# Optimization experiments

Hardware: AMD Instinct MI355X
Metric: run time of the kernel (lower is better)

Reference implementation:

```python
import jax, jax.numpy as jnp
import numpy as np

B, N, D, H = 16, 256, 128, 8
HD = D // H
PAIR_DIMS = [64, 64, 64]
EPS = 1e-8


def _pairwise_lv_fts(x):
    # x: [B, 4, N] four-vectors (px, py, pz, E); returns [B, N, N, 4] = (lnkt, lnz, lndelta, lnm2)
    px, py, pz, e = x[:, 0], x[:, 1], x[:, 2], x[:, 3]
    pt = jnp.sqrt(jnp.clip(px ** 2 + py ** 2, EPS))          # [B, N]
    rap = 0.5 * jnp.log1p(2.0 * pz / jnp.clip(e - pz, 1e-20))
    phi = jnp.arctan2(py, px)
    d_rap = rap[:, :, None] - rap[:, None, :]                 # [B, N, N]
    d_phi = (phi[:, :, None] - phi[:, None, :] + np.pi) % (2.0 * np.pi) - np.pi
    delta = jnp.sqrt(d_rap ** 2 + d_phi ** 2)
    lndelta = jnp.log(jnp.clip(delta, EPS))
    ptmin = jnp.minimum(pt[:, :, None], pt[:, None, :])
    lnkt = jnp.log(jnp.clip(ptmin * delta, EPS))
    lnz = jnp.log(jnp.clip(ptmin / jnp.clip(pt[:, :, None] + pt[:, None, :], EPS), EPS))
    es = e[:, :, None] + e[:, None, :]
    pxs = px[:, :, None] + px[:, None, :]
    pys = py[:, :, None] + py[:, None, :]
    pzs = pz[:, :, None] + pz[:, None, :]
    lnm2 = jnp.log(jnp.clip(es ** 2 - pxs ** 2 - pys ** 2 - pzs ** 2, EPS))
    return jnp.stack([lnkt, lnz, lndelta, lnm2], axis=-1)


def setup_inputs() -> dict:
    key = jax.random.key(0)
    ks = jax.random.split(key, 12)
    p3 = jax.random.normal(ks[0], (B, 3, N), jnp.float32)
    e = jnp.sqrt((p3 ** 2).sum(1, keepdims=True)
                 + jnp.abs(jax.random.normal(ks[1], (B, 1, N), jnp.float32)) ** 2 + 0.1)
    x_pf = jnp.concatenate([p3, e], axis=1)                   # physical four-vectors [B,4,N]
    x_feat = jax.random.normal(ks[2], (B, N, D), jnp.float32) * 0.02
    dims = [4] + PAIR_DIMS + [H]
    pw = {}
    for i in range(4):
        pw[f"pair_w{i}"] = jax.random.normal(ks[3 + i], (dims[i], dims[i + 1]), jnp.float32) / np.sqrt(dims[i])
        pw[f"pair_b{i}"] = jnp.zeros((dims[i + 1],), jnp.float32)
    proj = {n: jax.random.normal(k, (D, D), jnp.float32) / np.sqrt(D)
            for n, k in zip(["wq", "wk", "wv", "wo"], jax.random.split(ks[7], 4))}
    bias = {n: jnp.zeros((D,), jnp.float32) for n in ["bq", "bk", "bv", "bo"]}
    return dict(x_pf=x_pf, x_feat=x_feat, **pw, **proj, **bias)


def reference(x_pf, x_feat, pair_w0, pair_b0, pair_w1, pair_b1, pair_w2, pair_b2,
              pair_w3, pair_b3, wq, wk, wv, wo, bq, bk, bv, bo):
    # pairwise Lorentz-invariant features -> dense attention bias
    u = _pairwise_lv_fts(x_pf)                                # [B, N, N, 4]
    for w, b in ((pair_w0, pair_b0), (pair_w1, pair_b1), (pair_w2, pair_b2)):
        u = jax.nn.gelu(u @ w + b)
    attn_bias = jnp.transpose(u @ pair_w3 + pair_b3, (0, 3, 1, 2))  # [B, H, N, N]
    # multi-head attention with pairwise bias
    q = (x_feat @ wq + bq).reshape(B, N, H, HD)
    k = (x_feat @ wk + bk).reshape(B, N, H, HD)
    v = (x_feat @ wv + bv).reshape(B, N, H, HD)
    scores = jnp.einsum("bihd,bjhd->bhij", q, k) / np.sqrt(HD) + attn_bias
    attn = jax.nn.softmax(scores, axis=-1)
    out = jnp.einsum("bhij,bjhd->bihd", attn, v).reshape(B, N, D)
    return out @ wo + bo                                      # [B, N, D]
```

## Files before the change

### kernel.cpp

```cpp
#include <hip/hip_runtime.h>
#include <hip/hip_bf16.h>
#include <math.h>

#define B_ 16
#define N_ 256
#define D_ 128
#define H_ 8
#define HD_ 16
#define EPS_ 1e-8f
#define PI_F 3.14159265358979323846f
#define TWO_PI_F 6.28318530717958647692f
#define INV_TWO_PI_F 0.15915494309189533577f
#define L2E_F 1.4426950408889634f

#define OFF_PT   0
#define OFF_RAP  4096
#define OFF_PHI  8192
#define OFF_PX   12288
#define OFF_PY   16384
#define OFF_PZ   20480
#define OFF_E    24576
#define OFF_Q    28672
#define OFF_K    (28672 + 524288)
#define OFF_V    (28672 + 2*524288)
#define OFF_BIAS (28672 + 3*524288)
#define OFF_AO   (OFF_BIAS + 8388608)
#define OFF_WPACK (OFF_AO + 524288)

#define UA0  0
#define UA1H 2048
#define UA1L 6144
#define UA2H 10240
#define UA2L 14336
#define UA3H 18432
#define UA3L 19456
#define UQKV 20480

typedef _Float16 f16x8 __attribute__((ext_vector_type(8)));
typedef _Float16 f16x4 __attribute__((ext_vector_type(4)));
typedef _Float16 f16x2 __attribute__((ext_vector_type(2)));
typedef __attribute__((ext_vector_type(4))) float f4;
typedef __attribute__((ext_vector_type(4))) unsigned int u4;

__device__ __forceinline__ unsigned pkh2(float a, float b) {
    f16x2 v = { (_Float16)a, (_Float16)b };
    return __builtin_bit_cast(unsigned, v);
}
__device__ __forceinline__ float f16res(float x) {
    return x - (float)(_Float16)x;
}

__device__ __forceinline__ float gelu_f(float x) {
    float y2 = x * fmaf(0.10294337f, x * x, 2.3022079f);
    float e = __builtin_amdgcn_exp2f(-y2);
    return x * __builtin_amdgcn_rcpf(1.0f + e);
}


__global__ __launch_bounds__(256) void k_prep(
    const float* __restrict__ w0, const float* __restrict__ w1,
    const float* __restrict__ w2, const float* __restrict__ w3,
    const float* __restrict__ wq, const float* __restrict__ wk,
    const float* __restrict__ wv, const float* __restrict__ wo,
    _Float16* __restrict__ wp) {
    int id0 = blockIdx.x * 256 + threadIdx.x;
    int gs = gridDim.x * 256;
    for (int e = id0; e < 2048; e += gs) {
        int fi = e >> 3, j = e & 7;
        int mt = fi >> 6, lane = fi & 63;
        int q = lane >> 4, ln = lane & 15;
        int m = mt * 16 + ln;
        _Float16 v = (_Float16)0.0f;
        if (q == 0) v = (j < 4) ? (_Float16)w0[j * 64 + m]
                                : (_Float16)f16res(w0[(j - 4) * 64 + m]);
        else if (q == 1) v = (j < 4) ? (_Float16)w0[j * 64 + m] : (_Float16)0.0f;
        wp[UA0 + e] = v;
    }
    for (int e = id0; e < 4096; e += gs) {
        int fi = e >> 3, j = e & 7;
        int mt = fi >> 7, ks = (fi >> 6) & 1, lane = fi & 63;
        int q = lane >> 4;
        int m = mt * 16 + (lane & 15);
        int k = (2 * (j >> 2) + ks) * 16 + q * 4 + (j & 3);
        float x1 = w1[k * 64 + m];
        wp[UA1H + e] = (_Float16)x1;
        wp[UA1L + e] = (_Float16)f16res(x1);
        float x2 = w2[k * 64 + m];
        wp[UA2H + e] = (_Float16)x2;
        wp[UA2L + e] = (_Float16)f16res(x2);
    }
    for (int e = id0; e < 1024; e += gs) {
        int fi = e >> 3, j = e & 7;
        int ks = fi >> 6, lane = fi & 63;
        int q = lane >> 4;
        int m = lane & 15;
        int k = (2 * (j >> 2) + ks) * 16 + q * 4 + (j & 3);
        float x = (m < 8) ? w3[k * 8 + m] : 0.0f;
        wp[UA3H + e] = (_Float16)x;
        wp[UA3L + e] = (_Float16)f16res(x);
    }
    const float* mats[4] = { wq, wk, wv, wo };
#pragma unroll 1
    for (int mi = 0; mi < 4; ++mi) {
        const float* W = mats[mi];
        _Float16* dst = wp + UQKV + mi * 32768;
        for (int e = id0; e < 16384; e += gs) {
            int fi = e >> 3, j = e & 7;
            int mt = fi >> 8, ks = (fi >> 6) & 3, lane = fi & 63;
            int k = ks * 32 + ((lane >> 4) << 3) + j;
            int o = mt * 16 + (lane & 15);
            float x = W[k * 128 + o];
            dst[e] = (_Float16)x;
            dst[16384 + e] = (_Float16)f16res(x);
        }
    }
}

__global__ __launch_bounds__(256) void k_particle(const float* __restrict__ x_pf,
                                                  float* __restrict__ ws) {
    int idx = blockIdx.x * 256 + threadIdx.x;
    int b = idx >> 8, n = idx & 255;
    const float* base = x_pf + (size_t)b * 4 * N_;
    float px = base[0 * N_ + n];
    float py = base[1 * N_ + n];
    float pz = base[2 * N_ + n];
    float e  = base[3 * N_ + n];
    float pt  = sqrtf(fmaxf(px * px + py * py, EPS_));
    float rap = 0.5f * log1pf(2.0f * pz / fmaxf(e - pz, 1e-20f));
    float phi = atan2f(py, px);
    ws[OFF_PT  + idx] = pt;
    ws[OFF_RAP + idx] = rap;
    ws[OFF_PHI + idx] = phi;
    ws[OFF_PX  + idx] = px;
    ws[OFF_PY  + idx] = py;
    ws[OFF_PZ  + idx] = pz;
    ws[OFF_E   + idx] = e;
}

__device__ __forceinline__ void epi_frag(const f4 (&acc)[4][4], const float* __restrict__ bg,
                                         int q, u4 (&Bu)[4][2]) {
#pragma unroll
    for (int mt = 0; mt < 4; ++mt) {
        f4 bv = *(const f4*)&bg[mt * 16 + q * 4];
        int ks = mt & 1, hi = (mt >> 1) * 2;
#pragma unroll
        for (int nt = 0; nt < 4; ++nt) {
            float g0 = gelu_f(acc[mt][nt][0] + bv[0]);
            float g1 = gelu_f(acc[mt][nt][1] + bv[1]);
            float g2 = gelu_f(acc[mt][nt][2] + bv[2]);
            float g3 = gelu_f(acc[mt][nt][3] + bv[3]);
            Bu[nt][ks][hi]     = pkh2(g0, g1);
            Bu[nt][ks][hi + 1] = pkh2(g2, g3);
        }
    }
}

__device__ __forceinline__ void mid_layer(f4 (&acc)[4][4],
                                          const _Float16* __restrict__ wh,
                                          const _Float16* __restrict__ wl,
                                          int lane, const u4 (&Bu)[4][2]) {
    const f4 zero4 = { 0.f, 0.f, 0.f, 0.f };
#pragma unroll
    for (int mt = 0; mt < 4; ++mt) {
        f16x8 ah0 = *(const f16x8*)&wh[((mt * 2 + 0) * 64 + lane) * 8];
        f16x8 ah1 = *(const f16x8*)&wh[((mt * 2 + 1) * 64 + lane) * 8];
        f16x8 al0 = *(const f16x8*)&wl[((mt * 2 + 0) * 64 + lane) * 8];
        f16x8 al1 = *(const f16x8*)&wl[((mt * 2 + 1) * 64 + lane) * 8];
#pragma unroll
        for (int nt = 0; nt < 4; ++nt) {
            f16x8 b0 = __builtin_bit_cast(f16x8, Bu[nt][0]);
            f16x8 b1 = __builtin_bit_cast(f16x8, Bu[nt][1]);
            f4 c = zero4;
            c = __builtin_amdgcn_mfma_f32_16x16x32_f16(ah0, b0, c, 0, 0, 0);
            c = __builtin_amdgcn_mfma_f32_16x16x32_f16(al0, b0, c, 0, 0, 0);
            c = __builtin_amdgcn_mfma_f32_16x16x32_f16(ah1, b1, c, 0, 0, 0);
            c = __builtin_amdgcn_mfma_f32_16x16x32_f16(al1, b1, c, 0, 0, 0);
            acc[mt][nt] = c;
        }
    }
}

__global__ __launch_bounds__(256, 4) void k_pair_mlp(
    const float* __restrict__ ws, const _Float16* __restrict__ wp,
    const float* __restrict__ b0g, const float* __restrict__ b1g,
    const float* __restrict__ b2g, const float* __restrict__ b3g,
    float* __restrict__ bias_out) {
    int tid = threadIdx.x;
    int lane = tid & 63;
    int ln = lane & 15, q = lane >> 4;
    int wid = blockIdx.x * 4 + (tid >> 6);
    int row = wid >> 2;
    int j0 = (wid & 3) * 64;
    int b = row >> 8, i = row & 255;

    unsigned FH01, FH23, FL01, FL23;
    {
        int ib = row;
        int jb = (b << 8) + j0 + lane;
        float pt_i = ws[OFF_PT + ib],  rap_i = ws[OFF_RAP + ib], phi_i = ws[OFF_PHI + ib];
        float px_i = ws[OFF_PX + ib],  py_i  = ws[OFF_PY  + ib];
        float pz_i = ws[OFF_PZ + ib],  e_i   = ws[OFF_E   + ib];
        float pt_j = ws[OFF_PT + jb],  rap_j = ws[OFF_RAP + jb], phi_j = ws[OFF_PHI + jb];
        float px_j = ws[OFF_PX + jb],  py_j  = ws[OFF_PY  + jb];
        float pz_j = ws[OFF_PZ + jb],  e_j   = ws[OFF_E   + jb];

        float drap = rap_i - rap_j;
        float xw = phi_i - phi_j + PI_F;
        float mw = xw - TWO_PI_F * floorf(xw * INV_TWO_PI_F);
        float dphi = mw - PI_F;
        float delta = sqrtf(drap * drap + dphi * dphi);
        float f2 = __logf(fmaxf(delta, EPS_));
        float ptmin = fminf(pt_i, pt_j);
        float f0 = __logf(fmaxf(ptmin * delta, EPS_));
        float f1 = __logf(fmaxf(ptmin / fmaxf(pt_i + pt_j, EPS_), EPS_));
        float es = e_i + e_j, pxs = px_i + px_j, pys = py_i + py_j, pzs = pz_i + pz_j;
        float f3 = __logf(fmaxf(es * es - pxs * pxs - pys * pys - pzs * pzs, EPS_));

        FH01 = pkh2(f0, f1);
        FH23 = pkh2(f2, f3);
        FL01 = pkh2(f16res(f0), f16res(f1));
        FL23 = pkh2(f16res(f2), f16res(f3));
    }

    f4 acc[4][4];
    const f4 zero4 = { 0.f, 0.f, 0.f, 0.f };

    {
        f16x8 a0[4];
#pragma unroll
        for (int mt = 0; mt < 4; ++mt)
            a0[mt] = *(const f16x8*)&wp[UA0 + (mt * 64 + lane) * 8];
#pragma unroll
        for (int nt = 0; nt < 4; ++nt) {
            int src = nt * 16 + ln;
            unsigned h01 = (unsigned)__shfl((int)FH01, src);
            unsigned h23 = (unsigned)__shfl((int)FH23, src);
            unsigned l01 = (unsigned)__shfl((int)FL01, src);
            unsigned l23 = (unsigned)__shfl((int)FL23, src);
            u4 bu;
            bu[0] = (q == 0) ? h01 : ((q == 1) ? l01 : 0u);
            bu[1] = (q == 0) ? h23 : ((q == 1) ? l23 : 0u);
            bu[2] = (q == 0) ? h01 : 0u;
            bu[3] = (q == 0) ? h23 : 0u;
            f16x8 bf = __builtin_bit_cast(f16x8, bu);
#pragma unroll
            for (int mt = 0; mt < 4; ++mt)
                acc[mt][nt] = __builtin_amdgcn_mfma_f32_16x16x32_f16(a0[mt], bf, zero4, 0, 0, 0);
        }
    }

    u4 Bu[4][2];
    epi_frag(acc, b0g, q, Bu);
    mid_layer(acc, wp + UA1H, wp + UA1L, lane, Bu);
    epi_frag(acc, b1g, q, Bu);
    mid_layer(acc, wp + UA2H, wp + UA2L, lane, Bu);
    epi_frag(acc, b2g, q, Bu);

    {
        f16x8 a3h0 = *(const f16x8*)&wp[UA3H + (0 * 64 + lane) * 8];
        f16x8 a3h1 = *(const f16x8*)&wp[UA3H + (1 * 64 + lane) * 8];
        f16x8 a3l0 = *(const f16x8*)&wp[UA3L + (0 * 64 + lane) * 8];
        f16x8 a3l1 = *(const f16x8*)&wp[UA3L + (1 * 64 + lane) * 8];
        f4 acc3[4];
#pragma unroll
        for (int nt = 0; nt < 4; ++nt) {
            f16x8 b0 = __builtin_bit_cast(f16x8, Bu[nt][0]);
            f16x8 b1 = __builtin_bit_cast(f16x8, Bu[nt][1]);
            f4 c = zero4;
            c = __builtin_amdgcn_mfma_f32_16x16x32_f16(a3h0, b0, c, 0, 0, 0);
            c = __builtin_amdgcn_mfma_f32_16x16x32_f16(a3l0, b0, c, 0, 0, 0);
            c = __builtin_amdgcn_mfma_f32_16x16x32_f16(a3h1, b1, c, 0, 0, 0);
            c = __builtin_amdgcn_mfma_f32_16x16x32_f16(a3l1, b1, c, 0, 0, 0);
            acc3[nt] = c;
        }
        if (q < 2) {
            f4 b3v = *(const f4*)&b3g[q * 4];
#pragma unroll
            for (int nt = 0; nt < 4; ++nt) {
                int jc = j0 + nt * 16 + ln;
#pragma unroll
                for (int r = 0; r < 4; ++r) {
                    int out = q * 4 + r;
                    bias_out[(((size_t)(b * H_ + out)) * N_ + i) * N_ + jc] = acc3[nt][r] + b3v[r];
                }
            }
        }
    }
}

__device__ __forceinline__ void mfma_gemm64x16(
    const float* __restrict__ xrow,
    const _Float16* __restrict__ wpm,
    int mtbase,
    const float* __restrict__ biasv,
    float* __restrict__ outp,
    int lane) {
    int q = lane >> 4;
    const f4 zero4 = { 0.f, 0.f, 0.f, 0.f };
    f16x8 Bh[4], Bl[4];
#pragma unroll
    for (int ks = 0; ks < 4; ++ks) {
        const float* p = xrow + ks * 32 + q * 8;
        float4 xa = ((const float4*)p)[0];
        float4 xb = ((const float4*)p)[1];
        u4 hu = { pkh2(xa.x, xa.y), pkh2(xa.z, xa.w), pkh2(xb.x, xb.y), pkh2(xb.z, xb.w) };
        u4 lu = { pkh2(f16res(xa.x), f16res(xa.y)), pkh2(f16res(xa.z), f16res(xa.w)),
                  pkh2(f16res(xb.x), f16res(xb.y)), pkh2(f16res(xb.z), f16res(xb.w)) };
        Bh[ks] = __builtin_bit_cast(f16x8, hu);
        Bl[ks] = __builtin_bit_cast(f16x8, lu);
    }
#pragma unroll
    for (int mtl = 0; mtl < 4; ++mtl) {
        int mt = mtbase + mtl;
        f4 c = zero4;
#pragma unroll
        for (int ks = 0; ks < 4; ++ks) {
            const _Float16* fa = wpm + ((size_t)((mt * 4 + ks) * 64 + lane)) * 8;
            f16x8 ah = *(const f16x8*)fa;
            f16x8 al = *(const f16x8*)(fa + 16384);
            c = __builtin_amdgcn_mfma_f32_16x16x32_f16(ah, Bh[ks], c, 0, 0, 0);
            c = __builtin_amdgcn_mfma_f32_16x16x32_f16(ah, Bl[ks], c, 0, 0, 0);
            c = __builtin_amdgcn_mfma_f32_16x16x32_f16(al, Bh[ks], c, 0, 0, 0);
        }
        f4 bv = *(const f4*)&biasv[mtl * 16 + q * 4];
        f4 r = c + bv;
        *(f4*)(outp + mtl * 16 + q * 4) = r;
    }
}

__global__ __launch_bounds__(256) void k_qkv(
    const float* __restrict__ xf, const _Float16* __restrict__ wp,
    const float* __restrict__ bq, const float* __restrict__ bk, const float* __restrict__ bv,
    float* __restrict__ ws) {
    int tid = threadIdx.x;
    int lane = tid & 63, ln = lane & 15;
    int wid = blockIdx.x * 4 + (tid >> 6);
    int og = wid % 6, tg = wid / 6;
    int mi = og >> 1, ch = og & 1;
    const _Float16* wpm = wp + UQKV + mi * 32768;
    const float* bias = (mi == 0) ? bq : ((mi == 1) ? bk : bv);
    float* outb = ws + OFF_Q + (size_t)mi * 524288;
    size_t tok = (size_t)(tg * 16 + ln);
    mfma_gemm64x16(xf + tok * 128, wpm, ch * 4, bias + ch * 64,
                   outb + tok * 128 + ch * 64, lane);
}

#define SVT 264
__global__ __launch_bounds__(256) void k_attn(const float* __restrict__ ws,
                                              float* __restrict__ wso) {
    __shared__ __align__(16) _Float16 Vt[16 * SVT];
    int tid = threadIdx.x;
    int blk = blockIdx.x;
    int ib = blk & 3;
    int bh = blk >> 2;
    int b = bh >> 3, h = bh & 7;

    {
        const float* vr = ws + OFF_V + ((size_t)(b * 256 + tid)) * 128 + h * 16;
        float4 v0 = ((const float4*)vr)[0];
        float4 v1 = ((const float4*)vr)[1];
        float4 v2 = ((const float4*)vr)[2];
        float4 v3 = ((const float4*)vr)[3];
        Vt[ 0 * SVT + tid] = (_Float16)v0.x;  Vt[ 1 * SVT + tid] = (_Float16)v0.y;
        Vt[ 2 * SVT + tid] = (_Float16)v0.z;  Vt[ 3 * SVT + tid] = (_Float16)v0.w;
        Vt[ 4 * SVT + tid] = (_Float16)v1.x;  Vt[ 5 * SVT + tid] = (_Float16)v1.y;
        Vt[ 6 * SVT + tid] = (_Float16)v1.z;  Vt[ 7 * SVT + tid] = (_Float16)v1.w;
        Vt[ 8 * SVT + tid] = (_Float16)v2.x;  Vt[ 9 * SVT + tid] = (_Float16)v2.y;
        Vt[10 * SVT + tid] = (_Float16)v2.z;  Vt[11 * SVT + tid] = (_Float16)v2.w;
        Vt[12 * SVT + tid] = (_Float16)v3.x;  Vt[13 * SVT + tid] = (_Float16)v3.y;
        Vt[14 * SVT + tid] = (_Float16)v3.z;  Vt[15 * SVT + tid] = (_Float16)v3.w;
    }
    __syncthreads();

    int lane = tid & 63, w = tid >> 6;
    int ln = lane & 15, q = lane >> 4;
    int i0 = ib * 64 + w * 16;
    const f4 zero4 = { 0.f, 0.f, 0.f, 0.f };

    f16x8 Bq;
    {
        const float* qr = ws + OFF_Q + ((size_t)(b * 256 + i0 + ln)) * 128 + h * 16 + (q & 1) * 8;
        float4 qa = ((const float4*)qr)[0];
        float4 qb = ((const float4*)qr)[1];
        u4 hu = { pkh2(qa.x, qa.y), pkh2(qa.z, qa.w), pkh2(qb.x, qb.y), pkh2(qb.z, qb.w) };
        Bq = __builtin_bit_cast(f16x8, hu);
    }

    f4 accs[16];
    const float* Kbase = ws + OFF_K + ((size_t)(b * 256)) * 128 + h * 16;
    const float* bb = ws + OFF_BIAS + ((size_t)(bh * 256 + i0 + ln)) * 256 + q * 4;
#pragma unroll
    for (int mt = 0; mt < 16; ++mt) {
        const float* kr = Kbase + (size_t)(mt * 16 + ln) * 128 + (q & 1) * 8;
        float4 ka = ((const float4*)kr)[0];
        float4 kb = ((const float4*)kr)[1];
        u4 hu = { pkh2(ka.x, ka.y), pkh2(ka.z, ka.w), pkh2(kb.x, kb.y), pkh2(kb.z, kb.w) };
        u4 lu = { pkh2(f16res(ka.x), f16res(ka.y)), pkh2(f16res(ka.z), f16res(ka.w)),
                  pkh2(f16res(kb.x), f16res(kb.y)), pkh2(f16res(kb.z), f16res(kb.w)) };
        u4 au;
        bool qlo = (q < 2);
        au[0] = qlo ? hu[0] : lu[0];
        au[1] = qlo ? hu[1] : lu[1];
        au[2] = qlo ? hu[2] : lu[2];
        au[3] = qlo ? hu[3] : lu[3];
        f16x8 Ak = __builtin_bit_cast(f16x8, au);
        f4 s = __builtin_amdgcn_mfma_f32_16x16x32_f16(Ak, Bq, zero4, 0, 0, 0);
        f4 bias4 = *(const f4*)&bb[mt * 16];
#pragma unroll
        for (int r = 0; r < 4; ++r) s[r] = fmaf(s[r], 0.25f, bias4[r]);
        accs[mt] = s;
    }

    float mx = accs[0][0];
#pragma unroll
    for (int mt = 0; mt < 16; ++mt)
#pragma unroll
        for (int r = 0; r < 4; ++r) mx = fmaxf(mx, accs[mt][r]);
    mx = fmaxf(mx, __shfl_xor(mx, 16));
    mx = fmaxf(mx, __shfl_xor(mx, 32));
    float nms = -mx * L2E_F;
    float l = 0.0f;
#pragma unroll
    for (int mt = 0; mt < 16; ++mt) {
#pragma unroll
        for (int r = 0; r < 4; ++r) {
            float p = __builtin_amdgcn_exp2f(fmaf(accs[mt][r], L2E_F, nms));
            accs[mt][r] = p;
            l += p;
        }
    }
    l += __shfl_xor(l, 16);
    l += __shfl_xor(l, 32);
    float inv = __builtin_amdgcn_rcpf(l);

    f4 o = zero4;
#pragma unroll
    for (int ks = 0; ks < 8; ++ks) {
        u4 bp = { pkh2(accs[2 * ks][0], accs[2 * ks][1]),
                  pkh2(accs[2 * ks][2], accs[2 * ks][3]),
                  pkh2(accs[2 * ks + 1][0], accs[2 * ks + 1][1]),
                  pkh2(accs[2 * ks + 1][2], accs[2 * ks + 1][3]) };
        int vb = ln * SVT + 32 * ks + 4 * q;
        f16x4 lo4 = *(const f16x4*)&Vt[vb];
        f16x4 hi4 = *(const f16x4*)&Vt[vb + 16];
        f16x8 av;
        av[0] = lo4[0]; av[1] = lo4[1]; av[2] = lo4[2]; av[3] = lo4[3];
        av[4] = hi4[0]; av[5] = hi4[1]; av[6] = hi4[2]; av[7] = hi4[3];
        o = __builtin_amdgcn_mfma_f32_16x16x32_f16(av, __builtin_bit_cast(f16x8, bp), o, 0, 0, 0);
    }
    f4 res = o * inv;
    *(f4*)(wso + OFF_AO + ((size_t)(b * 256 + i0 + ln)) * 128 + h * 16 + q * 4) = res;
}

__global__ __launch_bounds__(256) void k_out(
    const float* __restrict__ ws, const _Float16* __restrict__ wp,
    const float* __restrict__ bo, float* __restrict__ out) {
    int tid = threadIdx.x;
    int lane = tid & 63, ln = lane & 15;
    int wid = blockIdx.x * 4 + (tid >> 6);
    int og = wid & 1, tg = wid >> 1;
    const _Float16* wpm = wp + UQKV + 3 * 32768;
    size_t tok = (size_t)(tg * 16 + ln);
    mfma_gemm64x16(ws + OFF_AO + tok * 128, wpm, og * 4, bo + og * 64,
                   out + tok * 128 + og * 64, lane);
}

extern "C" void kernel_launch(void* const* d_in, const int* in_sizes, int n_in,
                              void* d_out, int out_size, void* d_ws, size_t ws_size,
                              hipStream_t stream) {
    const float* x_pf   = (const float*)d_in[0];
    const float* x_feat = (const float*)d_in[1];
    const float* w0 = (const float*)d_in[2];
    const float* b0 = (const float*)d_in[3];
    const float* w1 = (const float*)d_in[4];
    const float* b1 = (const float*)d_in[5];
    const float* w2 = (const float*)d_in[6];
    const float* b2 = (const float*)d_in[7];
    const float* w3 = (const float*)d_in[8];
    const float* b3 = (const float*)d_in[9];
    const float* wq = (const float*)d_in[10];
    const float* wk = (const float*)d_in[11];
    const float* wv = (const float*)d_in[12];
    const float* wo = (const float*)d_in[13];
    const float* bq = (const float*)d_in[14];
    const float* bk = (const float*)d_in[15];
    const float* bv = (const float*)d_in[16];
    const float* bo = (const float*)d_in[17];
    float* ws  = (float*)d_ws;
    float* out = (float*)d_out;
    _Float16* wpack = (_Float16*)(ws + OFF_WPACK);

    hipLaunchKernelGGL(k_prep, dim3(64), dim3(256), 0, stream,
                       w0, w1, w2, w3, wq, wk, wv, wo, wpack);
    hipLaunchKernelGGL(k_particle, dim3(16), dim3(256), 0, stream, x_pf, ws);
    hipLaunchKernelGGL(k_pair_mlp, dim3(4096), dim3(256), 0, stream,
                       ws, wpack, b0, b1, b2, b3, ws + OFF_BIAS);
    hipLaunchKernelGGL(k_qkv, dim3(384), dim3(256), 0, stream,
                       x_feat, wpack, bq, bk, bv, ws);
    hipLaunchKernelGGL(k_attn, dim3(512), dim3(256), 0, stream, ws, ws);
    hipLaunchKernelGGL(k_out, dim3(128), dim3(256), 0, stream, ws, wpack, bo, out);
}
```

Measured before the change: 196.0 us.

## Exploit pair-feature symmetry and merge particle/prep and qkv/pair-MLP launches

The pairwise features are symmetric in (i,j), so the pair MLP now computes only upper-triangular 64-column tiles and writes each result to both (i,j) and (j,i) of the bias. This roughly halves the pair MLP work that dominates runtime. The particle kernel is folded into the prep kernel as extra blocks, and the QKV projection is folded into the pair-MLP launch as leading blocks, which removes two launches. The mirrored stores are column-strided and uncoalesced, and the diagonal tiles still compute the full block.

```diff
diff --git a/kernel.cpp b/kernel.cpp
--- a/kernel.cpp
+++ b/kernel.cpp
@@ -62,9 +62,30 @@
     const float* __restrict__ w2, const float* __restrict__ w3,
     const float* __restrict__ wq, const float* __restrict__ wk,
     const float* __restrict__ wv, const float* __restrict__ wo,
-    _Float16* __restrict__ wp) {
+    const float* __restrict__ x_pf,
+    _Float16* __restrict__ wp, float* __restrict__ ws) {
+    if (blockIdx.x >= 64) {
+        int idx = (blockIdx.x - 64) * 256 + threadIdx.x;
+        int b = idx >> 8, n = idx & 255;
+        const float* base = x_pf + (size_t)b * 4 * N_;
+        float px = base[0 * N_ + n];
+        float py = base[1 * N_ + n];
+        float pz = base[2 * N_ + n];
+        float e  = base[3 * N_ + n];
+        float pt  = sqrtf(fmaxf(px * px + py * py, EPS_));
+        float rap = 0.5f * log1pf(2.0f * pz / fmaxf(e - pz, 1e-20f));
+        float phi = atan2f(py, px);
+        ws[OFF_PT  + idx] = pt;
+        ws[OFF_RAP + idx] = rap;
+        ws[OFF_PHI + idx] = phi;
+        ws[OFF_PX  + idx] = px;
+        ws[OFF_PY  + idx] = py;
+        ws[OFF_PZ  + idx] = pz;
+        ws[OFF_E   + idx] = e;
+        return;
+    }
     int id0 = blockIdx.x * 256 + threadIdx.x;
-    int gs = gridDim.x * 256;
+    const int gs = 64 * 256;
     for (int e = id0; e < 2048; e += gs) {
         int fi = e >> 3, j = e & 7;
         int mt = fi >> 6, lane = fi & 63;
@@ -116,27 +137,6 @@
     }
 }
 
-__global__ __launch_bounds__(256) void k_particle(const float* __restrict__ x_pf,
-                                                  float* __restrict__ ws) {
-    int idx = blockIdx.x * 256 + threadIdx.x;
-    int b = idx >> 8, n = idx & 255;
-    const float* base = x_pf + (size_t)b * 4 * N_;
-    float px = base[0 * N_ + n];
-    float py = base[1 * N_ + n];
-    float pz = base[2 * N_ + n];
-    float e  = base[3 * N_ + n];
-    float pt  = sqrtf(fmaxf(px * px + py * py, EPS_));
-    float rap = 0.5f * log1pf(2.0f * pz / fmaxf(e - pz, 1e-20f));
-    float phi = atan2f(py, px);
-    ws[OFF_PT  + idx] = pt;
-    ws[OFF_RAP + idx] = rap;
-    ws[OFF_PHI + idx] = phi;
-    ws[OFF_PX  + idx] = px;
-    ws[OFF_PY  + idx] = py;
-    ws[OFF_PZ  + idx] = pz;
-    ws[OFF_E   + idx] = e;
-}
-
 __device__ __forceinline__ void epi_frag(const f4 (&acc)[4][4], const float* __restrict__ bg,
                                          int q, u4 (&Bu)[4][2]) {
 #pragma unroll
@@ -180,18 +180,79 @@
     }
 }
 
-__global__ __launch_bounds__(256, 4) void k_pair_mlp(
+__device__ __forceinline__ void mfma_gemm64x16(
+    const float* __restrict__ xrow, const _Float16* __restrict__ wpm,
+    int mtbase, const float* __restrict__ biasv, float* __restrict__ outp, int lane) {
+    int q = lane >> 4;
+    const f4 zero4 = { 0.f, 0.f, 0.f, 0.f };
+    f16x8 Bh[4], Bl[4];
+#pragma unroll
+    for (int ks = 0; ks < 4; ++ks) {
+        const float* p = xrow + ks * 32 + q * 8;
+        float4 xa = ((const float4*)p)[0];
+        float4 xb = ((const float4*)p)[1];
+        u4 hu = { pkh2(xa.x, xa.y), pkh2(xa.z, xa.w), pkh2(xb.x, xb.y), pkh2(xb.z, xb.w) };
+        u4 lu = { pkh2(f16res(xa.x), f16res(xa.y)), pkh2(f16res(xa.z), f16res(xa.w)),
+                  pkh2(f16res(xb.x), f16res(xb.y)), pkh2(f16res(xb.z), f16res(xb.w)) };
+        Bh[ks] = __builtin_bit_cast(f16x8, hu);
+        Bl[ks] = __builtin_bit_cast(f16x8, lu);
+    }
+#pragma unroll
+    for (int mtl = 0; mtl < 4; ++mtl) {
+        int mt = mtbase + mtl;
+        f4 c = zero4;
+#pragma unroll
+        for (int ks = 0; ks < 4; ++ks) {
+            const _Float16* fa = wpm + ((size_t)((mt * 4 + ks) * 64 + lane)) * 8;
+            f16x8 ah = *(const f16x8*)fa;
+            f16x8 al = *(const f16x8*)(fa + 16384);
+            c = __builtin_amdgcn_mfma_f32_16x16x32_f16(ah, Bh[ks], c, 0, 0, 0);
+            c = __builtin_amdgcn_mfma_f32_16x16x32_f16(ah, Bl[ks], c, 0, 0, 0);
+            c = __builtin_amdgcn_mfma_f32_16x16x32_f16(al, Bh[ks], c, 0, 0, 0);
+        }
+        f4 bv = *(const f4*)&biasv[mtl * 16 + q * 4];
+        f4 r = c + bv;
+        *(f4*)(outp + mtl * 16 + q * 4) = r;
+    }
+}
+
+__global__ __launch_bounds__(256, 4) void k_pair_qkv(
     const float* __restrict__ ws, const _Float16* __restrict__ wp,
     const float* __restrict__ b0g, const float* __restrict__ b1g,
     const float* __restrict__ b2g, const float* __restrict__ b3g,
-    float* __restrict__ bias_out) {
+    float* __restrict__ bias_out,
+    const float* __restrict__ xf,
+    const float* __restrict__ bqv, const float* __restrict__ bkv, const float* __restrict__ bvv,
+    float* __restrict__ qkv_out) {
     int tid = threadIdx.x;
     int lane = tid & 63;
     int ln = lane & 15, q = lane >> 4;
-    int wid = blockIdx.x * 4 + (tid >> 6);
-    int row = wid >> 2;
-    int j0 = (wid & 3) * 64;
-    int b = row >> 8, i = row & 255;
+
+    if (blockIdx.x < 384) {
+        int wid = blockIdx.x * 4 + (tid >> 6);
+        int og = wid % 6, tg = wid / 6;
+        int mi = og >> 1, ch = og & 1;
+        const _Float16* wpm = wp + UQKV + mi * 32768;
+        const float* bias = (mi == 0) ? bqv : ((mi == 1) ? bkv : bvv);
+        float* outb = qkv_out + OFF_Q + (size_t)mi * 524288;
+        size_t tok = (size_t)(tg * 16 + ln);
+        mfma_gemm64x16(xf + tok * 128, wpm, ch * 4, bias + ch * 64,
+                       outb + tok * 128 + ch * 64, lane);
+        return;
+    }
+
+    int w2 = (blockIdx.x - 384) * 4 + (tid >> 6);
+    int b = w2 / 640;
+    int w = w2 - b * 640;
+    int it, rr, nj;
+    if (w < 256)      { it = 0; rr = w;       nj = 4; }
+    else if (w < 448) { it = 1; rr = w - 256; nj = 3; }
+    else if (w < 576) { it = 2; rr = w - 448; nj = 2; }
+    else              { it = 3; rr = w - 576; nj = 1; }
+    int i  = it * 64 + rr / nj;
+    int jt = it + rr % nj;
+    int j0 = jt * 64;
+    int row = (b << 8) + i;
 
     unsigned FH01, FH23, FL01, FL23;
     {
@@ -275,74 +336,21 @@
         }
         if (q < 2) {
             f4 b3v = *(const f4*)&b3g[q * 4];
+            bool mirror = (jt != it);
 #pragma unroll
             for (int nt = 0; nt < 4; ++nt) {
                 int jc = j0 + nt * 16 + ln;
 #pragma unroll
                 for (int r = 0; r < 4; ++r) {
                     int out = q * 4 + r;
-                    bias_out[(((size_t)(b * H_ + out)) * N_ + i) * N_ + jc] = acc3[nt][r] + b3v[r];
+                    float val = acc3[nt][r] + b3v[r];
+                    size_t basebh = ((size_t)(b * H_ + out)) * N_;
+                    bias_out[(basebh + i) * N_ + jc] = val;
+                    if (mirror) bias_out[(basebh + jc) * N_ + i] = val;
                 }
             }
         }
     }
-}
-
-__device__ __forceinline__ void mfma_gemm64x16(
-    const float* __restrict__ xrow,
-    const _Float16* __restrict__ wpm,
-    int mtbase,
-    const float* __restrict__ biasv,
-    float* __restrict__ outp,
-    int lane) {
-    int q = lane >> 4;
-    const f4 zero4 = { 0.f, 0.f, 0.f, 0.f };
-    f16x8 Bh[4], Bl[4];
-#pragma unroll
-    for (int ks = 0; ks < 4; ++ks) {
-        const float* p = xrow + ks * 32 + q * 8;
-        float4 xa = ((const float4*)p)[0];
-        float4 xb = ((const float4*)p)[1];
-        u4 hu = { pkh2(xa.x, xa.y), pkh2(xa.z, xa.w), pkh2(xb.x, xb.y), pkh2(xb.z, xb.w) };
-        u4 lu = { pkh2(f16res(xa.x), f16res(xa.y)), pkh2(f16res(xa.z), f16res(xa.w)),
-                  pkh2(f16res(xb.x), f16res(xb.y)), pkh2(f16res(xb.z), f16res(xb.w)) };
-        Bh[ks] = __builtin_bit_cast(f16x8, hu);
-        Bl[ks] = __builtin_bit_cast(f16x8, lu);
-    }
-#pragma unroll
-    for (int mtl = 0; mtl < 4; ++mtl) {
-        int mt = mtbase + mtl;
-        f4 c = zero4;
-#pragma unroll
-        for (int ks = 0; ks < 4; ++ks) {
-            const _Float16* fa = wpm + ((size_t)((mt * 4 + ks) * 64 + lane)) * 8;
-            f16x8 ah = *(const f16x8*)fa;
-            f16x8 al = *(const f16x8*)(fa + 16384);
-            c = __builtin_amdgcn_mfma_f32_16x16x32_f16(ah, Bh[ks], c, 0, 0, 0);
-            c = __builtin_amdgcn_mfma_f32_16x16x32_f16(ah, Bl[ks], c, 0, 0, 0);
-            c = __builtin_amdgcn_mfma_f32_16x16x32_f16(al, Bh[ks], c, 0, 0, 0);
-        }
-        f4 bv = *(const f4*)&biasv[mtl * 16 + q * 4];
-        f4 r = c + bv;
-        *(f4*)(outp + mtl * 16 + q * 4) = r;
-    }
-}
-
-__global__ __launch_bounds__(256) void k_qkv(
-    const float* __restrict__ xf, const _Float16* __restrict__ wp,
-    const float* __restrict__ bq, const float* __restrict__ bk, const float* __restrict__ bv,
-    float* __restrict__ ws) {
-    int tid = threadIdx.x;
-    int lane = tid & 63, ln = lane & 15;
-    int wid = blockIdx.x * 4 + (tid >> 6);
-    int og = wid % 6, tg = wid / 6;
-    int mi = og >> 1, ch = og & 1;
-    const _Float16* wpm = wp + UQKV + mi * 32768;
-    const float* bias = (mi == 0) ? bq : ((mi == 1) ? bk : bv);
-    float* outb = ws + OFF_Q + (size_t)mi * 524288;
-    size_t tok = (size_t)(tg * 16 + ln);
-    mfma_gemm64x16(xf + tok * 128, wpm, ch * 4, bias + ch * 64,
-                   outb + tok * 128 + ch * 64, lane);
 }
 
 #define SVT 264
@@ -490,13 +498,11 @@
     float* out = (float*)d_out;
     _Float16* wpack = (_Float16*)(ws + OFF_WPACK);
 
-    hipLaunchKernelGGL(k_prep, dim3(64), dim3(256), 0, stream,
-                       w0, w1, w2, w3, wq, wk, wv, wo, wpack);
-    hipLaunchKernelGGL(k_particle, dim3(16), dim3(256), 0, stream, x_pf, ws);
-    hipLaunchKernelGGL(k_pair_mlp, dim3(4096), dim3(256), 0, stream,
-                       ws, wpack, b0, b1, b2, b3, ws + OFF_BIAS);
-    hipLaunchKernelGGL(k_qkv, dim3(384), dim3(256), 0, stream,
-                       x_feat, wpack, bq, bk, bv, ws);
+    hipLaunchKernelGGL(k_prep, dim3(80), dim3(256), 0, stream,
+                       w0, w1, w2, w3, wq, wk, wv, wo, x_pf, wpack, ws);
+    hipLaunchKernelGGL(k_pair_qkv, dim3(384 + 2560), dim3(256), 0, stream,
+                       ws, wpack, b0, b1, b2, b3, ws + OFF_BIAS,
+                       x_feat, bq, bk, bv, ws);
     hipLaunchKernelGGL(k_attn, dim3(512), dim3(256), 0, stream, ws, ws);
     hipLaunchKernelGGL(k_out, dim3(128), dim3(256), 0, stream, ws, wpack, bo, out);
 }
```

Result: faster. 174.8 us (-10.8%).
